# Kernel tuning notes

Measured on AMD Instinct MI355X. Metric: run time of the kernel, lower is better.

## Reference

```python
import jax, jax.numpy as jnp
import numpy as np

B, S, D = 16, 2048, 1024


def setup_inputs() -> dict:
    key = jax.random.key(0)
    ks = jax.random.split(key, 12)
    s = 1.0 / np.sqrt(D)
    s2 = 1.0 / np.sqrt(4 * D)
    return {
        "token_embeddings": jax.random.normal(ks[0], (B, S, D), dtype=jnp.float32),
        "attention_mask": jax.random.randint(ks[1], (B, S), 0, 2, dtype=jnp.int32),
        # linear weights stored as [in, out]
        "Wq": jax.random.uniform(ks[2], (D, D), jnp.float32, -s, s),
        "bq": jnp.zeros((D,), jnp.float32),
        "Wk": jax.random.uniform(ks[3], (D, D), jnp.float32, -s, s),
        "bk": jnp.zeros((D,), jnp.float32),
        "Wv": jax.random.uniform(ks[4], (D, D), jnp.float32, -s, s),
        "bv": jnp.zeros((D,), jnp.float32),
        "W1": jax.random.uniform(ks[5], (D, 4 * D), jnp.float32, -s, s),
        "b1": jnp.zeros((4 * D,), jnp.float32),
        "W2": jax.random.uniform(ks[6], (4 * D, D), jnp.float32, -s2, s2),
        "b2": jnp.zeros((D,), jnp.float32),
    }


def reference(token_embeddings, attention_mask, Wq, bq, Wk, bk, Wv, bv, W1, b1, W2, b2):
    d = token_embeddings.shape[-1]
    q = token_embeddings @ Wq + bq          # [B,S,D]
    k = token_embeddings @ Wk + bk          # [B,S,D]
    v = token_embeddings @ Wv + bv          # [B,S,D]
    scores = jnp.einsum("bqd,bkd->bqk", q, k) / jnp.sqrt(jnp.float32(d))  # [B,S,S]
    scores = jnp.where(attention_mask[:, None, :] == 0, -jnp.inf, scores)
    weights = jax.nn.softmax(scores, axis=-1)
    attn = jnp.einsum("bqk,bkd->bqd", weights, v)  # [B,S,D]
    pooled = attn.mean(axis=1)                      # [B,D]
    h = jax.nn.relu(pooled @ W1 + b1)               # [B,4D]
    return jnp.tanh(h @ W2 + b2)                    # [B,D]
```

## Files before the change

### kernel.cpp

```cpp
#include <hip/hip_runtime.h>
#include <hip/hip_bf16.h>

constexpr int B_ = 16;
constexpr int S_ = 2048;
constexpr int D_ = 1024;
constexpr int C_ = 1280;
constexpr long long BSD = (long long)B_ * S_ * D_;

typedef unsigned short u16;
typedef __bf16 bf16x8 __attribute__((ext_vector_type(8)));
typedef float    f32x4 __attribute__((ext_vector_type(4)));
typedef unsigned short usx8 __attribute__((ext_vector_type(8)));
typedef unsigned short usx4 __attribute__((ext_vector_type(4)));

__device__ inline u16 f2b(float f) {
  unsigned u = __float_as_uint(f);
  u = (u + 0x7fffu + ((u >> 16) & 1u)) >> 16;
  return (u16)u;
}
__device__ inline float b2f(u16 v) { return __uint_as_float(((unsigned)v) << 16); }

__device__ __forceinline__ void gll16(const void* g, void* l) {
  __builtin_amdgcn_global_load_lds(
      (const __attribute__((address_space(1))) void*)g,
      (__attribute__((address_space(3))) void*)l, 16, 0, 0);
}

__device__ __forceinline__ void vmwait4() {
  asm volatile("s_waitcnt vmcnt(4)" ::: "memory");
  __builtin_amdgcn_sched_barrier(0);
}
__device__ __forceinline__ void vmwait2() {
  asm volatile("s_waitcnt vmcnt(2)" ::: "memory");
  __builtin_amdgcn_sched_barrier(0);
}
__device__ __forceinline__ void vmwait0() {
  asm volatile("s_waitcnt vmcnt(0)" ::: "memory");
  __builtin_amdgcn_sched_barrier(0);
}
__device__ __forceinline__ void lgkm0w() {
  asm volatile("s_waitcnt lgkmcnt(0)" ::: "memory");
  __builtin_amdgcn_sched_barrier(0);
}
__device__ __forceinline__ void barrier_pin() {
  __builtin_amdgcn_sched_barrier(0);
  __builtin_amdgcn_s_barrier();
  __builtin_amdgcn_sched_barrier(0);
}

__global__ __launch_bounds__(256) void k_prep(
    const float* __restrict__ X, u16* __restrict__ Xb,
    const float* __restrict__ Wq, const float* __restrict__ Wk, const float* __restrict__ Wv,
    const float* __restrict__ bq, const float* __restrict__ bk, const float* __restrict__ bv,
    const int* __restrict__ mask, u16* __restrict__ Wt,
    float* __restrict__ biasQKV, int* __restrict__ map, int* __restrict__ counts) {
  __shared__ float tile[32][33];
  __shared__ int ts[256];
  const int bid = blockIdx.x;
  const int tid = threadIdx.x;
  if (bid < 16384) {
    size_t i = ((size_t)bid * 256 + tid) * 8;
    f32x4 a = *(const f32x4*)(X + i);
    f32x4 b = *(const f32x4*)(X + i + 4);
    usx8 o;
    o[0] = f2b(a[0]); o[1] = f2b(a[1]); o[2] = f2b(a[2]); o[3] = f2b(a[3]);
    o[4] = f2b(b[0]); o[5] = f2b(b[1]); o[6] = f2b(b[2]); o[7] = f2b(b[3]);
    *(usx8*)(Xb + i) = o;
  } else if (bid < 16384 + 3072) {
    const int wb = bid - 16384;
    const int z = wb >> 10, t = wb & 1023;
    const float* W = (z == 0) ? Wq : (z == 1 ? Wk : Wv);
    u16* dst = Wt + (size_t)z * D_ * D_;
    const int n0 = (t & 31) * 32, k0 = (t >> 5) * 32;
    const int tx = tid & 31, ty = tid >> 5;
    for (int r = ty; r < 32; r += 8)
      tile[r][tx] = W[(size_t)(k0 + r) * D_ + n0 + tx];
    __syncthreads();
    for (int r = ty; r < 32; r += 8)
      dst[(size_t)(n0 + r) * D_ + k0 + tx] = f2b(tile[tx][r]);
  } else if (bid == 16384 + 3072) {
    for (int x = tid; x < 3072; x += 256)
      biasQKV[x] = (x < 1024) ? bq[x] : (x < 2048 ? bk[x - 1024] : bv[x - 2048]);
  } else {
    const int b = bid - (16384 + 3073);
    const int* mrow = mask + b * S_;
    int lv[8]; int s = 0;
#pragma unroll
    for (int j = 0; j < 8; ++j) { lv[j] = (mrow[tid * 8 + j] != 0) ? 1 : 0; s += lv[j]; }
    ts[tid] = s;
    __syncthreads();
    for (int off = 1; off < 256; off <<= 1) {
      int v = (tid >= off) ? ts[tid - off] : 0;
      __syncthreads();
      ts[tid] += v;
      __syncthreads();
    }
    int pos = ts[tid] - s;
#pragma unroll
    for (int j = 0; j < 8; ++j) if (lv[j]) map[b * C_ + (pos++)] = tid * 8 + j;
    const int nb = ts[255];
    if (tid == 0) counts[b] = nb;
    for (int x = nb + tid; x < C_; x += 256) map[b * C_ + x] = 0;
  }
}

#define READ_A(DD, MQ)                                                    \
  _Pragma("unroll")                                                       \
  for (int f = 0; f < 4; ++f) {                                           \
    const int ad = (DD) + (MQ) * 8192 + A_pre + f * 1024;                 \
    a_[f][0] = *(const bf16x8*)(sm + ad);                                 \
    a_[f][1] = *(const bf16x8*)(sm + (ad ^ 32));                          \
  }

#define READ_B(DD, NQ)                                                    \
  _Pragma("unroll")                                                       \
  for (int n = 0; n < 2; ++n) {                                           \
    const int bd = (DD) + 16384 + (NQ) * 8192 + B_pre + n * 1024;         \
    b_[NQ][n][0] = *(const bf16x8*)(sm + bd);                             \
    b_[NQ][n][1] = *(const bf16x8*)(sm + (bd ^ 32));                      \
  }

#define MFMA_Q(IO, JO, BQ)                                                \
  __builtin_amdgcn_s_setprio(1);                                         \
  _Pragma("unroll")                                                       \
  for (int kk = 0; kk < 2; ++kk)                                          \
    _Pragma("unroll")                                                     \
    for (int f = 0; f < 4; ++f)                                           \
      _Pragma("unroll")                                                   \
      for (int n = 0; n < 2; ++n)                                         \
        acc[(IO) + f][(JO) + n] = __builtin_amdgcn_mfma_f32_16x16x32_bf16(\
            a_[f][kk], b_[BQ][n][kk], acc[(IO) + f][(JO) + n], 0, 0, 0);  \
  __builtin_amdgcn_s_setprio(0);

template <int MODE>
__global__ __launch_bounds__(512, 2) void k_gemm8(
    const u16* __restrict__ A, const u16* __restrict__ Bt,
    const float* __restrict__ bias, u16* __restrict__ C,
    const int* __restrict__ map, const int* __restrict__ counts, float scale) {
  extern __shared__ u16 sm[];
  constexpr int NT = 16;
  const int tid = threadIdx.x, lane = tid & 63, wave = tid >> 6;

  const int gx = gridDim.x, gy = gridDim.y;
  const int nwg = gx * gy * gridDim.z;
  const int orig = blockIdx.x + gx * (blockIdx.y + gy * blockIdx.z);
  const int cpx = nwg >> 3;
  const int tl = (orig & 7) * cpx + (orig >> 3);
  const int bx = tl % gx;
  const int rest = tl / gx;
  const int by = rest % gy;
  const int bz = rest / gy;

  const u16* Az; const u16* Bz;
  int batch = 0, mtile = 0;
  if constexpr (MODE == 0) { Az = A; Bz = Bt; }
  else if constexpr (MODE == 1) {
    batch = by / 5; mtile = by - batch * 5;
    if (mtile * 256 >= counts[batch]) return;
    Az = A + (size_t)batch * S_ * D_; Bz = Bt;
  } else {
    batch = bz;
    if (bx * 256 >= counts[batch]) return;
    Az = A + (size_t)batch * S_ * D_;
    Bz = Bt + (size_t)batch * C_ * D_;
  }
  const int wm_i = wave >> 2, wn_i = wave & 3;
  const int n0 = bx * 256;

  const int grow = tid >> 3;
  const int gslot = ((tid & 7) ^ ((tid >> 3) & 7)) * 8;
  const u16 *pAa0, *pAb0, *pAa1, *pAb1;
  if constexpr (MODE == 1) {
    const int* mp = map + batch * C_ + mtile * 256;
    pAa0 = Az + (size_t)mp[grow] * D_ + gslot;
    pAb0 = Az + (size_t)mp[grow + 64] * D_ + gslot;
    pAa1 = Az + (size_t)mp[grow + 128] * D_ + gslot;
    pAb1 = Az + (size_t)mp[grow + 192] * D_ + gslot;
  } else {
    const int m0 = by * 256;
    pAa0 = Az + (size_t)(m0 + grow) * D_ + gslot;
    pAb0 = pAa0 + (size_t)64 * D_;
    pAa1 = pAa0 + (size_t)128 * D_;
    pAb1 = pAa0 + (size_t)192 * D_;
  }
  const u16* pBa0 = Bz + (size_t)(n0 + grow) * D_ + gslot;
  const u16* pBb0 = pBa0 + (size_t)64 * D_;
  const u16* pBa1 = pBa0 + (size_t)128 * D_;
  const u16* pBb1 = pBa0 + (size_t)192 * D_;

  auto stage_part = [&](int t, int part) {
    const u16* ga = (part == 0) ? pAa0 : (part == 1) ? pAa1 : (part == 2) ? pBa0 : pBa1;
    const u16* gb = (part == 0) ? pAb0 : (part == 1) ? pAb1 : (part == 2) ? pBb0 : pBb1;
    u16* l0 = sm + (t & 1) * 32768 + part * 8192 + wave * 512;
    gll16(ga + t * 64, l0);
    gll16(gb + t * 64, l0 + 4096);
  };

  const int r16 = lane & 15;
  const int s0k = (lane >> 4) ^ (lane & 7);
  const int A_pre = wm_i * 4096 + r16 * 64 + s0k * 8;
  const int B_pre = wn_i * 2048 + r16 * 64 + s0k * 8;

  f32x4 acc[8][4] = {};
  bf16x8 a_[4][2], b_[2][2][2];

  stage_part(0, 0); stage_part(0, 2); stage_part(0, 3); stage_part(0, 1);
  vmwait4();
  barrier_pin();

#pragma unroll 1
  for (int t = 0; t < NT - 1; ++t) {
    const int DD = (t & 1) * 32768;
    READ_A(DD, 0) READ_B(DD, 0)
    __builtin_amdgcn_sched_barrier(0);
    stage_part(t + 1, 0);
    vmwait4(); barrier_pin(); lgkm0w();
    MFMA_Q(0, 0, 0)
    barrier_pin();
    READ_B(DD, 1)
    __builtin_amdgcn_sched_barrier(0);
    stage_part(t + 1, 2);
    vmwait4(); barrier_pin(); lgkm0w();
    MFMA_Q(0, 2, 1)
    barrier_pin();
    READ_A(DD, 1)
    __builtin_amdgcn_sched_barrier(0);
    stage_part(t + 1, 3);
    barrier_pin(); lgkm0w();
    MFMA_Q(4, 2, 1)
    barrier_pin();
    stage_part(t + 1, 1);
    vmwait4(); barrier_pin();
    MFMA_Q(4, 0, 0)
    barrier_pin();
  }
  {
    const int DD = ((NT - 1) & 1) * 32768;
    READ_A(DD, 0) READ_B(DD, 0)
    vmwait2(); barrier_pin(); lgkm0w();
    MFMA_Q(0, 0, 0)
    barrier_pin();
    READ_B(DD, 1)
    vmwait0(); barrier_pin(); lgkm0w();
    MFMA_Q(0, 2, 1)
    barrier_pin();
    READ_A(DD, 1)
    barrier_pin(); lgkm0w();
    MFMA_Q(4, 2, 1)
    barrier_pin();
    MFMA_Q(4, 0, 0)
  }

#pragma unroll
  for (int i = 0; i < 8; ++i) {
    const int MQ = i >> 2, f = i & 3;
    const int lrow = MQ * 128 + wm_i * 64 + f * 16 + ((lane >> 4) << 2);
#pragma unroll
    for (int j = 0; j < 4; ++j) {
      const int NQ = j >> 1, n = j & 1;
      const int col = n0 + NQ * 128 + wn_i * 32 + n * 16 + (lane & 15);
      if constexpr (MODE == 0) {
        const float badd = bias[col];
        u16* cp = C + (size_t)(by * 256 + lrow) * 1024 + col;
#pragma unroll
        for (int r = 0; r < 4; ++r) cp[(size_t)r * 1024] = f2b(acc[i][j][r] + badd);
      } else if constexpr (MODE == 1) {
        const float badd = bias[1024 + col];
        u16* cp = C + (size_t)(col >> 10) * ((size_t)16 * C_ * 1024)
                    + ((size_t)batch * C_ + mtile * 256 + lrow) * 1024 + (col & 1023);
#pragma unroll
        for (int r = 0; r < 4; ++r) cp[(size_t)r * 1024] = f2b(acc[i][j][r] + badd);
      } else {
        u16* cp = C + ((size_t)batch * 2048 + by * 256 + lrow) * C_ + col;
#pragma unroll
        for (int r = 0; r < 4; ++r) cp[(size_t)r * C_] = f2b(acc[i][j][r] * scale);
      }
    }
  }
}

__global__ __launch_bounds__(256) void k_softmax_colsum(
    const u16* __restrict__ Sc, const int* __restrict__ counts,
    float* __restrict__ cpart) {
  __shared__ float colsum[C_];
  const int b = blockIdx.y, bi = blockIdx.x;
  const int tid = threadIdx.x, lane = tid & 63, wave = tid >> 6;
  for (int k = tid; k < C_; k += 256) colsum[k] = 0.0f;
  __syncthreads();

  const int nb = counts[b];
  const u16* base = Sc + ((size_t)b * 2048 + bi * 64 + wave * 16) * C_;
  const int c16 = lane * 16;
  const int c4 = 1024 + lane * 4;
  float csum[20];
#pragma unroll
  for (int i = 0; i < 20; i++) csum[i] = 0.0f;

  for (int rr = 0; rr < 16; rr++) {
    const u16* srow = base + (size_t)rr * C_;
    usx8 x0 = *(const usx8*)(srow + c16);
    usx8 x1 = *(const usx8*)(srow + c16 + 8);
    usx4 x2 = *(const usx4*)(srow + c4);
    float s[20];
    float m = -1e30f;
#pragma unroll
    for (int e = 0; e < 8; e++) {
      s[e] = (c16 + e < nb) ? b2f(x0[e]) : -1e30f;
      s[8 + e] = (c16 + 8 + e < nb) ? b2f(x1[e]) : -1e30f;
      m = fmaxf(m, fmaxf(s[e], s[8 + e]));
    }
#pragma unroll
    for (int e = 0; e < 4; e++) {
      s[16 + e] = (c4 + e < nb) ? b2f(x2[e]) : -1e30f;
      m = fmaxf(m, s[16 + e]);
    }
#pragma unroll
    for (int o = 1; o < 64; o <<= 1) m = fmaxf(m, __shfl_xor(m, o));
    float sum = 0.f;
#pragma unroll
    for (int i = 0; i < 20; i++) { s[i] = __expf(s[i] - m); sum += s[i]; }
#pragma unroll
    for (int o = 1; o < 64; o <<= 1) sum += __shfl_xor(sum, o);
    const float inv = 1.0f / (sum * (float)S_);
#pragma unroll
    for (int i = 0; i < 20; i++) csum[i] += s[i] * inv;
  }
#pragma unroll
  for (int i = 0; i < 16; i++) {
    const int e = (i + lane) & 15;
    atomicAdd(&colsum[c16 + e], csum[e]);
  }
#pragma unroll
  for (int i = 0; i < 4; i++) {
    const int e = (i + lane) & 3;
    atomicAdd(&colsum[c4 + e], csum[16 + e]);
  }
  __syncthreads();
  float* dst = cpart + ((size_t)b * 32 + bi) * C_;
  for (int k = tid; k < C_; k += 256) dst[k] = colsum[k];
}

__global__ __launch_bounds__(256) void k_cv(const float* __restrict__ cpart,
                                            const u16* __restrict__ Vc,
                                            float* __restrict__ pooled) {
  __shared__ float cl[128];
  const int b = blockIdx.y;
  const int k0 = blockIdx.x * 128;
  const int tid = threadIdx.x;
  if (tid < 128) {
    float s = 0.f;
    const float* p = cpart + (size_t)b * 32 * C_ + k0 + tid;
#pragma unroll 4
    for (int q = 0; q < 32; q++) s += p[(size_t)q * C_];
    cl[tid] = s;
  }
  __syncthreads();
  f32x4 acc = {};
  const u16* vb = Vc + ((size_t)b * C_ + k0) * 1024 + tid * 4;
  for (int k = 0; k < 128; k++) {
    const float w = cl[k];
    usx4 v = *(const usx4*)(vb + (size_t)k * 1024);
    acc[0] += w * b2f(v[0]);
    acc[1] += w * b2f(v[1]);
    acc[2] += w * b2f(v[2]);
    acc[3] += w * b2f(v[3]);
  }
#pragma unroll
  for (int q = 0; q < 4; q++) atomicAdd(&pooled[b * D_ + tid * 4 + q], acc[q]);
}

__global__ __launch_bounds__(256) void k_mlp1(const float* __restrict__ pooled,
                                              const float* __restrict__ W1,
                                              float* __restrict__ hpre) {
  __shared__ float ps[16][256];
  const int tid = threadIdx.x;
  const int j = blockIdx.x * 256 + tid;
  const int i0 = blockIdx.y * 256;
  for (int x = tid; x < 16 * 256; x += 256) {
    const int bb = x >> 8, ii = x & 255;
    ps[bb][ii] = pooled[bb * D_ + i0 + ii];
  }
  __syncthreads();
  float acc[16] = {};
  for (int i = 0; i < 256; i++) {
    const float w = W1[(size_t)(i0 + i) * (4 * D_) + j];
#pragma unroll
    for (int bb = 0; bb < 16; bb++) acc[bb] += ps[bb][i] * w;
  }
#pragma unroll
  for (int bb = 0; bb < 16; bb++) atomicAdd(&hpre[bb * (4 * D_) + j], acc[bb]);
}

__global__ __launch_bounds__(256) void k_mlp2(const float* __restrict__ hpre,
                                              const float* __restrict__ b1,
                                              const float* __restrict__ W2,
                                              float* __restrict__ outpre) {
  __shared__ float hs[16][256];
  const int tid = threadIdx.x;
  const int n = blockIdx.x * 256 + tid;
  const int i0 = blockIdx.y * 256;
  for (int x = tid; x < 16 * 256; x += 256) {
    const int bb = x >> 8, ii = x & 255;
    hs[bb][ii] = fmaxf(hpre[bb * (4 * D_) + i0 + ii] + b1[i0 + ii], 0.0f);
  }
  __syncthreads();
  float acc[16] = {};
  for (int i = 0; i < 256; i++) {
    const float w = W2[(size_t)(i0 + i) * D_ + n];
#pragma unroll
    for (int bb = 0; bb < 16; bb++) acc[bb] += hs[bb][i] * w;
  }
#pragma unroll
  for (int bb = 0; bb < 16; bb++) atomicAdd(&outpre[bb * D_ + n], acc[bb]);
}

__global__ void k_finish(const float* __restrict__ outpre, const float* __restrict__ b2,
                         float* __restrict__ out) {
  const int x = blockIdx.x * 256 + threadIdx.x;
  out[x] = tanhf(outpre[x] + b2[x & (D_ - 1)]);
}

extern "C" void kernel_launch(void* const* d_in, const int* in_sizes, int n_in,
                              void* d_out, int out_size, void* d_ws, size_t ws_size,
                              hipStream_t stream) {
  const float* X  = (const float*)d_in[0];
  const int* mask = (const int*)d_in[1];
  const float* Wq = (const float*)d_in[2];
  const float* bq = (const float*)d_in[3];
  const float* Wk = (const float*)d_in[4];
  const float* bk = (const float*)d_in[5];
  const float* Wv = (const float*)d_in[6];
  const float* bv = (const float*)d_in[7];
  const float* W1 = (const float*)d_in[8];
  const float* b1 = (const float*)d_in[9];
  const float* W2 = (const float*)d_in[10];
  const float* b2 = (const float*)d_in[11];
  float* out = (float*)d_out;

  char* ws = (char*)d_ws;
  size_t off = 0;
  auto alloc = [&](size_t bytes) -> void* {
    void* p = ws + off;
    off += (bytes + 255) & ~(size_t)255;
    return p;
  };
  u16* Qb  = (u16*)alloc(BSD * sizeof(u16));
  u16* KVc = (u16*)alloc((size_t)2 * 16 * C_ * D_ * sizeof(u16));
  u16* Kc  = KVc;
  u16* Vc  = KVc + (size_t)16 * C_ * D_;
  u16* ScX = (u16*)alloc((size_t)16 * 2048 * C_ * sizeof(u16));
  u16* Xb  = ScX;
  u16* Sc  = ScX;
  u16* Wt  = (u16*)alloc((size_t)3 * D_ * D_ * sizeof(u16));
  float* biasQKV = (float*)alloc(3 * D_ * sizeof(float));
  int* map    = (int*)alloc((size_t)16 * C_ * sizeof(int));
  int* counts = (int*)alloc(16 * sizeof(int));
  float* cpart  = (float*)alloc((size_t)32 * 16 * C_ * sizeof(float));
  float* pooled = (float*)alloc((size_t)B_ * D_ * sizeof(float));
  float* hpre   = (float*)alloc((size_t)B_ * 4 * D_ * sizeof(float));
  float* outpre = (float*)alloc((size_t)B_ * D_ * sizeof(float));
  (void)ws_size; (void)in_sizes; (void)n_in; (void)out_size;

  const size_t zero_bytes = (size_t)B_ * D_ * 4 + (size_t)B_ * 4 * D_ * 4 +
                            (size_t)B_ * D_ * 4;
  hipMemsetAsync(pooled, 0, zero_bytes, stream);

  k_prep<<<16384 + 3089, 256, 0, stream>>>(X, Xb, Wq, Wk, Wv, bq, bk, bv,
                                           mask, Wt, biasQKV, map, counts);

  k_gemm8<0><<<dim3(4, 128, 1), 512, 131072, stream>>>(
      Xb, Wt, biasQKV, Qb, nullptr, nullptr, 1.0f);

  k_gemm8<1><<<dim3(8, 16 * (C_ / 256), 1), 512, 131072, stream>>>(
      Xb, Wt + (size_t)D_ * D_, biasQKV, KVc, map, counts, 1.0f);

  k_gemm8<2><<<dim3(C_ / 256, 8, 16), 512, 131072, stream>>>(
      Qb, Kc, nullptr, Sc, nullptr, counts, 0.03125f);

  k_softmax_colsum<<<dim3(32, B_), 256, 0, stream>>>(Sc, counts, cpart);
  k_cv<<<dim3(C_ / 128, B_), 256, 0, stream>>>(cpart, Vc, pooled);
  k_mlp1<<<dim3(16, 4), 256, 0, stream>>>(pooled, W1, hpre);
  k_mlp2<<<dim3(4, 16), 256, 0, stream>>>(hpre, b1, W2, outpre);
  k_finish<<<64, 256, 0, stream>>>(outpre, b2, out);
}
```

Baseline: 446.0 us.

## Merge Q and compacted KV projections into one launch, simplify load pipeline

Fuses the Q projection GEMM and the gathered K/V projection GEMM into a single launch of 1152 workgroups, each taking the Q or KV role from its remapped tile index. This removes one launch and the tail gap between the two GEMMs. The kernel's prefetch schedule also changes: the staggered per-part loads with partial vmcnt waits become all four parts issued at once with a full vmcnt(0) wait before the last MFMA quarter. Load interleaving is coarser, which may expose more memory latency, and the mixed tile types can leave the work unevenly balanced.

```diff
diff --git a/kernel.cpp b/kernel.cpp
--- a/kernel.cpp
+++ b/kernel.cpp
@@ -26,14 +26,6 @@
       (__attribute__((address_space(3))) void*)l, 16, 0, 0);
 }
 
-__device__ __forceinline__ void vmwait4() {
-  asm volatile("s_waitcnt vmcnt(4)" ::: "memory");
-  __builtin_amdgcn_sched_barrier(0);
-}
-__device__ __forceinline__ void vmwait2() {
-  asm volatile("s_waitcnt vmcnt(2)" ::: "memory");
-  __builtin_amdgcn_sched_barrier(0);
-}
 __device__ __forceinline__ void vmwait0() {
   asm volatile("s_waitcnt vmcnt(0)" ::: "memory");
   __builtin_amdgcn_sched_barrier(0);
@@ -135,7 +127,7 @@
 template <int MODE>
 __global__ __launch_bounds__(512, 2) void k_gemm8(
     const u16* __restrict__ A, const u16* __restrict__ Bt,
-    const float* __restrict__ bias, u16* __restrict__ C,
+    const float* __restrict__ bias, u16* __restrict__ C, u16* __restrict__ C2,
     const int* __restrict__ map, const int* __restrict__ counts, float scale) {
   extern __shared__ u16 sm[];
   constexpr int NT = 16;
@@ -146,20 +138,28 @@
   const int orig = blockIdx.x + gx * (blockIdx.y + gy * blockIdx.z);
   const int cpx = nwg >> 3;
   const int tl = (orig & 7) * cpx + (orig >> 3);
-  const int bx = tl % gx;
-  const int rest = tl / gx;
-  const int by = rest % gy;
-  const int bz = rest / gy;
 
   const u16* Az; const u16* Bz;
-  int batch = 0, mtile = 0;
-  if constexpr (MODE == 0) { Az = A; Bz = Bt; }
-  else if constexpr (MODE == 1) {
-    batch = by / 5; mtile = by - batch * 5;
-    if (mtile * 256 >= counts[batch]) return;
-    Az = A + (size_t)batch * S_ * D_; Bz = Bt;
+  int batch = 0, mtile = 0, bx, by;
+  bool isQ = false;
+  if constexpr (MODE == 0) {
+    if (tl < 512) {
+      isQ = true;
+      bx = tl & 3; by = tl >> 2;
+      Az = A; Bz = Bt;
+    } else {
+      const int i = tl - 512;
+      bx = i & 7; by = i >> 3;
+      batch = by / 5; mtile = by - batch * 5;
+      if (mtile * 256 >= counts[batch]) return;
+      Az = A + (size_t)batch * S_ * D_;
+      Bz = Bt + (size_t)D_ * D_;
+    }
   } else {
-    batch = bz;
+    bx = tl % gx;
+    const int rest = tl / gx;
+    by = rest % gy;
+    batch = rest / gy;
     if (bx * 256 >= counts[batch]) return;
     Az = A + (size_t)batch * S_ * D_;
     Bz = Bt + (size_t)batch * C_ * D_;
@@ -170,7 +170,7 @@
   const int grow = tid >> 3;
   const int gslot = ((tid & 7) ^ ((tid >> 3) & 7)) * 8;
   const u16 *pAa0, *pAb0, *pAa1, *pAb1;
-  if constexpr (MODE == 1) {
+  if (MODE == 0 && !isQ) {
     const int* mp = map + batch * C_ + mtile * 256;
     pAa0 = Az + (size_t)mp[grow] * D_ + gslot;
     pAb0 = Az + (size_t)mp[grow + 64] * D_ + gslot;
@@ -195,6 +195,9 @@
     gll16(ga + t * 64, l0);
     gll16(gb + t * 64, l0 + 4096);
   };
+  auto stage_all = [&](int t) {
+    stage_part(t, 0); stage_part(t, 1); stage_part(t, 2); stage_part(t, 3);
+  };
 
   const int r16 = lane & 15;
   const int s0k = (lane >> 4) ^ (lane & 7);
@@ -204,8 +207,8 @@
   f32x4 acc[8][4] = {};
   bf16x8 a_[4][2], b_[2][2][2];
 
-  stage_part(0, 0); stage_part(0, 2); stage_part(0, 3); stage_part(0, 1);
-  vmwait4();
+  stage_all(0);
+  vmwait0();
   barrier_pin();
 
 #pragma unroll 1
@@ -213,35 +216,30 @@
     const int DD = (t & 1) * 32768;
     READ_A(DD, 0) READ_B(DD, 0)
     __builtin_amdgcn_sched_barrier(0);
-    stage_part(t + 1, 0);
-    vmwait4(); barrier_pin(); lgkm0w();
+    stage_all(t + 1);
+    barrier_pin(); lgkm0w();
     MFMA_Q(0, 0, 0)
     barrier_pin();
     READ_B(DD, 1)
-    __builtin_amdgcn_sched_barrier(0);
-    stage_part(t + 1, 2);
-    vmwait4(); barrier_pin(); lgkm0w();
+    barrier_pin(); lgkm0w();
     MFMA_Q(0, 2, 1)
     barrier_pin();
     READ_A(DD, 1)
-    __builtin_amdgcn_sched_barrier(0);
-    stage_part(t + 1, 3);
     barrier_pin(); lgkm0w();
     MFMA_Q(4, 2, 1)
     barrier_pin();
-    stage_part(t + 1, 1);
-    vmwait4(); barrier_pin();
+    vmwait0(); barrier_pin();
     MFMA_Q(4, 0, 0)
     barrier_pin();
   }
   {
     const int DD = ((NT - 1) & 1) * 32768;
     READ_A(DD, 0) READ_B(DD, 0)
-    vmwait2(); barrier_pin(); lgkm0w();
+    barrier_pin(); lgkm0w();
     MFMA_Q(0, 0, 0)
     barrier_pin();
     READ_B(DD, 1)
-    vmwait0(); barrier_pin(); lgkm0w();
+    barrier_pin(); lgkm0w();
     MFMA_Q(0, 2, 1)
     barrier_pin();
     READ_A(DD, 1)
@@ -260,16 +258,18 @@
       const int NQ = j >> 1, n = j & 1;
       const int col = n0 + NQ * 128 + wn_i * 32 + n * 16 + (lane & 15);
       if constexpr (MODE == 0) {
-        const float badd = bias[col];
-        u16* cp = C + (size_t)(by * 256 + lrow) * 1024 + col;
-#pragma unroll
-        for (int r = 0; r < 4; ++r) cp[(size_t)r * 1024] = f2b(acc[i][j][r] + badd);
-      } else if constexpr (MODE == 1) {
-        const float badd = bias[1024 + col];
-        u16* cp = C + (size_t)(col >> 10) * ((size_t)16 * C_ * 1024)
-                    + ((size_t)batch * C_ + mtile * 256 + lrow) * 1024 + (col & 1023);
-#pragma unroll
-        for (int r = 0; r < 4; ++r) cp[(size_t)r * 1024] = f2b(acc[i][j][r] + badd);
+        if (isQ) {
+          const float badd = bias[col];
+          u16* cp = C + (size_t)(by * 256 + lrow) * 1024 + col;
+#pragma unroll
+          for (int r = 0; r < 4; ++r) cp[(size_t)r * 1024] = f2b(acc[i][j][r] + badd);
+        } else {
+          const float badd = bias[1024 + col];
+          u16* cp = C2 + (size_t)(col >> 10) * ((size_t)16 * C_ * 1024)
+                      + ((size_t)batch * C_ + mtile * 256 + lrow) * 1024 + (col & 1023);
+#pragma unroll
+          for (int r = 0; r < 4; ++r) cp[(size_t)r * 1024] = f2b(acc[i][j][r] + badd);
+        }
       } else {
         u16* cp = C + ((size_t)batch * 2048 + by * 256 + lrow) * C_ + col;
 #pragma unroll
@@ -468,14 +468,11 @@
   k_prep<<<16384 + 3089, 256, 0, stream>>>(X, Xb, Wq, Wk, Wv, bq, bk, bv,
                                            mask, Wt, biasQKV, map, counts);
 
-  k_gemm8<0><<<dim3(4, 128, 1), 512, 131072, stream>>>(
-      Xb, Wt, biasQKV, Qb, nullptr, nullptr, 1.0f);
-
-  k_gemm8<1><<<dim3(8, 16 * (C_ / 256), 1), 512, 131072, stream>>>(
-      Xb, Wt + (size_t)D_ * D_, biasQKV, KVc, map, counts, 1.0f);
+  k_gemm8<0><<<dim3(1152, 1, 1), 512, 131072, stream>>>(
+      Xb, Wt, biasQKV, Qb, KVc, map, counts, 1.0f);
 
   k_gemm8<2><<<dim3(C_ / 256, 8, 16), 512, 131072, stream>>>(
-      Qb, Kc, nullptr, Sc, nullptr, counts, 0.03125f);
+      Qb, Kc, nullptr, Sc, nullptr, nullptr, counts, 0.03125f);
 
   k_softmax_colsum<<<dim3(32, B_), 256, 0, stream>>>(Sc, counts, cpart);
   k_cv<<<dim3(C_ / 128, B_), 256, 0, stream>>>(cpart, Vc, pooled);
```

Result: slower. 468.7 us (+5.1%).
